# Performance work log

Measured on AMD Instinct MI355X. Metric: run time of the kernel, lower is better.

## Reference

```python
import jax, jax.numpy as jnp
import numpy as np

MAX_L = 6
L = MAX_L + 1  # internal self.max_l in the torch module
N = 2_000_000


def _sph_constants(Lmax):
    lm = np.arange(Lmax)
    ls = lm * lm
    pt = np.zeros((Lmax, Lmax), dtype=np.int64)
    yr = np.zeros((Lmax, Lmax), dtype=np.int64)
    yr_rev = np.zeros((Lmax, Lmax), dtype=np.int64)
    num_lm = (Lmax + 1) * Lmax // 2
    ca = np.zeros(num_lm, dtype=np.float64)
    cb = np.zeros(num_lm, dtype=np.float64)
    for l in range(Lmax):
        m = np.arange(l + 1)
        pt[l, : l + 1] = m + l * (l + 1) // 2
        yr[l, : l + 1] = ls[l] + l + m
        yr_rev[l, : l + 1] = ls[l] + l - m
        if l > 0:
            ca[pt[l, :l]] = np.sqrt((4.0 * ls[l] - 1.0) / (ls[l] - ls[:l]))
            cb[pt[l, :l]] = -np.sqrt((ls[l - 1] - ls[:l]) / (4.0 * ls[l - 1] - 1.0))
    p1 = -np.sqrt(1.0 + 0.5 / np.maximum(lm, 1))  # prefactor1; index 0 unused
    p2 = np.sqrt(2.0 * lm + 3.0)                  # prefactor2
    return pt, yr, yr_rev, ca, cb, p1, p2

_PT, _YR, _YRR, _CA, _CB, _P1, _P2 = _sph_constants(L)
_SQRT2_REV = float(np.sqrt(0.5))
_SQRT2PI_REV = float(np.sqrt(0.5 / np.pi))
_HC1 = float(np.sqrt(15.0 / (4.0 * np.pi)))
_HC2 = float(np.sqrt(5.0 / (16.0 * np.pi)))
_HC3 = float(np.sqrt(15.0 / (16.0 * np.pi)))


def setup_inputs() -> dict:
    key = jax.random.key(0)
    cart = jax.random.normal(key, (3, N), dtype=jnp.float32)
    return {"cart": cart}


def _sph_forward(cart):
    dt = cart.dtype
    x, y, z = cart[0], cart[1], cart[2]
    d_sq = x * x + y * y + z * z  # == norm(cart, axis=0)**2
    nb = x.ndim  # number of trailing batch dims (here 1)

    sph = [None] * (L * L)
    sph[0] = jnp.full(x.shape, _SQRT2PI_REV * _SQRT2_REV, dtype=dt)
    sph[1] = (_P1[1] * _SQRT2PI_REV) * y
    sph[2] = (_P2[0] * _SQRT2_REV * _SQRT2PI_REV) * z
    sph[3] = (_P1[1] * _SQRT2PI_REV) * x
    # l = 2 hard-coded block
    sph[4] = _HC1 * x * y
    sph[5] = -_HC1 * y * z
    sph[6] = _HC2 * (3.0 * z * z - d_sq)
    sph[7] = -_HC1 * x * z
    sph[8] = _HC3 * (x * x - y * y)

    for l in range(3, L):
        # vectorized band over m = 0..l-2 (positive-m / yr branch)
        a = jnp.asarray(_CA[_PT[l, : l - 1]], dt).reshape((l - 1,) + (1,) * nb)
        b = jnp.asarray(_CB[_PT[l, : l - 1]], dt).reshape((l - 1,) + (1,) * nb)
        prev = jnp.stack([sph[int(_YR[l - 1, m])] for m in range(l - 1)])
        prev2 = jnp.stack([sph[int(_YR[l - 2, m])] for m in range(l - 1)])
        blk = a * (z * prev + b * d_sq * prev2)
        for m in range(l - 1):
            sph[int(_YR[l, m])] = blk[m]
        # negative-m / yr_rev branch over m = 1..l-2
        if l - 1 > 1:
            a2 = jnp.asarray(_CA[_PT[l, 1 : l - 1]], dt).reshape((l - 2,) + (1,) * nb)
            b2 = jnp.asarray(_CB[_PT[l, 1 : l - 1]], dt).reshape((l - 2,) + (1,) * nb)
            prev_r = jnp.stack([sph[int(_YRR[l - 1, m])] for m in range(1, l - 1)])
            prev2_r = jnp.stack([sph[int(_YRR[l - 2, m])] for m in range(1, l - 1)])
            blk_r = a2 * (z * prev_r + b2 * d_sq * prev2_r)
            for i, m in enumerate(range(1, l - 1)):
                sph[int(_YRR[l, m])] = blk_r[i]
        # edge terms m = l-1 and m = l
        top_p = sph[int(_YR[l - 1, l - 1])]
        top_n = sph[int(_YRR[l - 1, l - 1])]
        sph[int(_YR[l, l - 1])] = _P2[l - 1] * z * top_p
        sph[int(_YRR[l, l - 1])] = _P2[l - 1] * z * top_n
        sph[int(_YR[l, l])] = _P1[l] * (x * top_p - y * top_n)
        sph[int(_YRR[l, l])] = _P1[l] * (x * top_n + y * top_p)

    return jnp.stack(sph)  # (L*L, ...batch)


def reference(cart):
    return _sph_forward(cart)
```

## Files before the change

kernel.cpp:

```cpp
#include <hip/hip_runtime.h>

constexpr double csqrt(double x) {
    double r = x > 1.0 ? x : 1.0;
    for (int i = 0; i < 60; ++i) r = 0.5 * (r + x / r);
    return r;
}

constexpr double PI_D    = 3.14159265358979323846264338327950288;
constexpr double SQ2R    = csqrt(0.5);
constexpr double SQ2PIR  = csqrt(0.5 / PI_D);
constexpr double C00_D   = SQ2PIR * SQ2R;
constexpr double C1Y_D   = -csqrt(1.5) * SQ2PIR;
constexpr double C1Z_D   = csqrt(3.0) * SQ2R * SQ2PIR;
constexpr double HC1_D   = csqrt(15.0 / (4.0 * PI_D));
constexpr double HC2_D   = csqrt(5.0 / (16.0 * PI_D));
constexpr double HC3_D   = csqrt(15.0 / (16.0 * PI_D));

struct SphConsts {
    double ca[7][7];
    double cb[7][7];
    double p1[7];
    double p2[7];
};

constexpr SphConsts makeConsts() {
    SphConsts c{};
    for (int l = 1; l < 7; ++l) {
        for (int m = 0; m < l; ++m) {
            c.ca[l][m] = csqrt((4.0 * l * l - 1.0) / (double)(l * l - m * m));
            double num = (double)((l - 1) * (l - 1) - m * m);
            double den = 4.0 * (l - 1) * (l - 1) - 1.0;
            c.cb[l][m] = -csqrt(num / den < 0.0 ? 0.0 : num / den);
        }
        c.p1[l] = -csqrt(1.0 + 0.5 / (double)l);
    }
    for (int l = 0; l < 7; ++l) c.p2[l] = csqrt(2.0 * l + 3.0);
    return c;
}

constexpr SphConsts CC = makeConsts();

typedef float f2 __attribute__((ext_vector_type(2)));

__device__ __forceinline__ void stv(float* p, float v) {
    __builtin_nontemporal_store(v, p);
}
__device__ __forceinline__ void stv(float* p, f2 v) {
    __builtin_nontemporal_store(v, reinterpret_cast<f2*>(p));
}

template <typename T> __device__ __forceinline__ T bcast(float v);
template <> __device__ __forceinline__ float bcast<float>(float v) { return v; }
template <> __device__ __forceinline__ f2    bcast<f2>(float v)    { f2 t = {v, v}; return t; }

template <typename T>
__device__ __forceinline__ void sph_point(T X, T Y, T Z, float* __restrict__ o, size_t N) {
    const T D = X * X + Y * Y + Z * Z;

    stv(o, bcast<T>((float)C00_D));
    T b1_0 = (float)C1Y_D * Y;
    T b1_1 = (float)C1Z_D * Z;
    T b1_2 = (float)C1Y_D * X;
    stv(o + 1 * N, b1_0);
    stv(o + 2 * N, b1_1);
    stv(o + 3 * N, b1_2);
    T b2_0 = (float)HC1_D * (X * Y);
    T b2_1 = (float)(-HC1_D) * (Y * Z);
    T b2_2 = (float)HC2_D * (3.0f * (Z * Z) - D);
    T b2_3 = (float)(-HC1_D) * (X * Z);
    T b2_4 = (float)HC3_D * (X * X - Y * Y);
    stv(o + 4 * N, b2_0);
    stv(o + 5 * N, b2_1);
    stv(o + 6 * N, b2_2);
    stv(o + 7 * N, b2_3);
    stv(o + 8 * N, b2_4);

    T prev2[13], prev[13], cur[13];
    prev2[0] = b1_0; prev2[1] = b1_1; prev2[2] = b1_2;
    prev[0] = b2_0; prev[1] = b2_1; prev[2] = b2_2; prev[3] = b2_3; prev[4] = b2_4;

#pragma unroll
    for (int l = 3; l <= 6; ++l) {
#pragma unroll
        for (int m = 0; m <= l - 2; ++m) {
            const float a = (float)CC.ca[l][m];
            const float b = (float)CC.cb[l][m];
            cur[l + m] = a * (Z * prev[(l - 1) + m] + b * (D * prev2[(l - 2) + m]));
        }
#pragma unroll
        for (int m = 1; m <= l - 2; ++m) {
            const float a = (float)CC.ca[l][m];
            const float b = (float)CC.cb[l][m];
            cur[l - m] = a * (Z * prev[(l - 1) - m] + b * (D * prev2[(l - 2) - m]));
        }
        const T top_p = prev[2 * l - 2];
        const T top_n = prev[0];
        const float p2v = (float)CC.p2[l - 1];
        const float p1v = (float)CC.p1[l];
        cur[2 * l - 1] = p2v * (Z * top_p);
        cur[1]         = p2v * (Z * top_n);
        cur[2 * l]     = p1v * (X * top_p - Y * top_n);
        cur[0]         = p1v * (X * top_n + Y * top_p);

#pragma unroll
        for (int j = 0; j <= 2 * l; ++j)
            stv(o + (size_t)(l * l + j) * N, cur[j]);

#pragma unroll
        for (int j = 0; j < 2 * l - 1; ++j) prev2[j] = prev[j];
#pragma unroll
        for (int j = 0; j < 2 * l + 1; ++j) prev[j] = cur[j];
    }
}

template <typename T, int W>
__global__ void sph_kernel(const float* __restrict__ cart,
                           float* __restrict__ out, int N) {
    const int i = blockIdx.x * blockDim.x + threadIdx.x;
    const int nW = N / W;
    if (i >= nW) return;
    const size_t sN = (size_t)N;
    const float* p = cart + (size_t)W * i;
    T X = *reinterpret_cast<const T*>(p);
    T Y = *reinterpret_cast<const T*>(p + sN);
    T Z = *reinterpret_cast<const T*>(p + 2 * sN);
    sph_point<T>(X, Y, Z, out + (size_t)W * i, sN);
}

extern "C" void kernel_launch(void* const* d_in, const int* in_sizes, int n_in,
                              void* d_out, int out_size, void* d_ws, size_t ws_size,
                              hipStream_t stream) {
    const float* cart = (const float*)d_in[0];
    float* out = (float*)d_out;
    const int N = in_sizes[0] / 3;

    const int threads = 256;
    if ((N & 1) == 0) {
        const int n2 = N >> 1;
        const int blocks = (n2 + threads - 1) / threads;
        sph_kernel<f2, 2><<<blocks, threads, 0, stream>>>(cart, out, N);
    } else {
        const int blocks = (N + threads - 1) / threads;
        sph_kernel<float, 1><<<blocks, threads, 0, stream>>>(cart, out, N);
    }
}
```

Before: 77.51 us.

## Reorder recurrence by m-columns and widen to float4 per thread

```diff
diff --git a/kernel.cpp b/kernel.cpp
--- a/kernel.cpp
+++ b/kernel.cpp
@@ -11,10 +11,6 @@
 constexpr double SQ2PIR  = csqrt(0.5 / PI_D);
 constexpr double C00_D   = SQ2PIR * SQ2R;
 constexpr double C1Y_D   = -csqrt(1.5) * SQ2PIR;
-constexpr double C1Z_D   = csqrt(3.0) * SQ2R * SQ2PIR;
-constexpr double HC1_D   = csqrt(15.0 / (4.0 * PI_D));
-constexpr double HC2_D   = csqrt(5.0 / (16.0 * PI_D));
-constexpr double HC3_D   = csqrt(15.0 / (16.0 * PI_D));
 
 struct SphConsts {
     double ca[7][7];
@@ -40,76 +36,73 @@
 
 constexpr SphConsts CC = makeConsts();
 
-typedef float f2 __attribute__((ext_vector_type(2)));
+typedef float f4 __attribute__((ext_vector_type(4)));
 
 __device__ __forceinline__ void stv(float* p, float v) {
     __builtin_nontemporal_store(v, p);
 }
-__device__ __forceinline__ void stv(float* p, f2 v) {
-    __builtin_nontemporal_store(v, reinterpret_cast<f2*>(p));
+__device__ __forceinline__ void stv(float* p, f4 v) {
+    __builtin_nontemporal_store(v, reinterpret_cast<f4*>(p));
 }
 
 template <typename T> __device__ __forceinline__ T bcast(float v);
 template <> __device__ __forceinline__ float bcast<float>(float v) { return v; }
-template <> __device__ __forceinline__ f2    bcast<f2>(float v)    { f2 t = {v, v}; return t; }
+template <> __device__ __forceinline__ f4    bcast<f4>(float v)    { f4 t = {v, v, v, v}; return t; }
 
 template <typename T>
-__device__ __forceinline__ void sph_point(T X, T Y, T Z, float* __restrict__ o, size_t N) {
-    const T D = X * X + Y * Y + Z * Z;
+__device__ __forceinline__ void sph_point(T x, T y, T z, float* __restrict__ o, size_t N) {
+    const T d2 = x * x + y * y + z * z;
 
-    stv(o, bcast<T>((float)C00_D));
-    T b1_0 = (float)C1Y_D * Y;
-    T b1_1 = (float)C1Z_D * Z;
-    T b1_2 = (float)C1Y_D * X;
-    stv(o + 1 * N, b1_0);
-    stv(o + 2 * N, b1_1);
-    stv(o + 3 * N, b1_2);
-    T b2_0 = (float)HC1_D * (X * Y);
-    T b2_1 = (float)(-HC1_D) * (Y * Z);
-    T b2_2 = (float)HC2_D * (3.0f * (Z * Z) - D);
-    T b2_3 = (float)(-HC1_D) * (X * Z);
-    T b2_4 = (float)HC3_D * (X * X - Y * Y);
-    stv(o + 4 * N, b2_0);
-    stv(o + 5 * N, b2_1);
-    stv(o + 6 * N, b2_2);
-    stv(o + 7 * N, b2_3);
-    stv(o + 8 * N, b2_4);
+    T pa = bcast<T>((float)C00_D);
+    stv(o + 0 * N, pa);
+    T pb = (float)CC.p2[0] * (z * pa);
+    stv(o + 2 * N, pb);
+#pragma unroll
+    for (int l = 2; l <= 6; ++l) {
+        const float a = (float)CC.ca[l][0];
+        const float b = (float)CC.cb[l][0];
+        T pc = a * (z * pb + b * (d2 * pa));
+        stv(o + (size_t)(l * l + l) * N, pc);
+        pa = pb; pb = pc;
+    }
 
-    T prev2[13], prev[13], cur[13];
-    prev2[0] = b1_0; prev2[1] = b1_1; prev2[2] = b1_2;
-    prev[0] = b2_0; prev[1] = b2_1; prev[2] = b2_2; prev[3] = b2_3; prev[4] = b2_4;
+    T dp = (float)C1Y_D * x;
+    T dn = (float)C1Y_D * y;
+    stv(o + 3 * N, dp);
+    stv(o + 1 * N, dn);
 
 #pragma unroll
-    for (int l = 3; l <= 6; ++l) {
+    for (int m = 1; m <= 6; ++m) {
+        if (m >= 2) {
+            const float p1v = (float)CC.p1[m];
+            T ndp = p1v * (x * dp - y * dn);
+            T ndn = p1v * (x * dn + y * dp);
+            dp = ndp; dn = ndn;
+            stv(o + (size_t)(m * m + 2 * m) * N, dp);
+            stv(o + (size_t)(m * m) * N, dn);
+        }
+        if (m <= 5) {
+            const float p2v = (float)CC.p2[m];
+            T qp = p2v * (z * dp);
+            T qn = p2v * (z * dn);
+            {
+                const int l = m + 1;
+                stv(o + (size_t)(l * l + l + m) * N, qp);
+                stv(o + (size_t)(l * l + l - m) * N, qn);
+            }
+            T ap = dp, bp = qp, an = dn, bn = qn;
 #pragma unroll
-        for (int m = 0; m <= l - 2; ++m) {
-            const float a = (float)CC.ca[l][m];
-            const float b = (float)CC.cb[l][m];
-            cur[l + m] = a * (Z * prev[(l - 1) + m] + b * (D * prev2[(l - 2) + m]));
+            for (int l = m + 2; l <= 6; ++l) {
+                const float a = (float)CC.ca[l][m];
+                const float b = (float)CC.cb[l][m];
+                T cp = a * (z * bp + b * (d2 * ap));
+                T cn = a * (z * bn + b * (d2 * an));
+                stv(o + (size_t)(l * l + l + m) * N, cp);
+                stv(o + (size_t)(l * l + l - m) * N, cn);
+                ap = bp; bp = cp;
+                an = bn; bn = cn;
+            }
         }
-#pragma unroll
-        for (int m = 1; m <= l - 2; ++m) {
-            const float a = (float)CC.ca[l][m];
-            const float b = (float)CC.cb[l][m];
-            cur[l - m] = a * (Z * prev[(l - 1) - m] + b * (D * prev2[(l - 2) - m]));
-        }
-        const T top_p = prev[2 * l - 2];
-        const T top_n = prev[0];
-        const float p2v = (float)CC.p2[l - 1];
-        const float p1v = (float)CC.p1[l];
-        cur[2 * l - 1] = p2v * (Z * top_p);
-        cur[1]         = p2v * (Z * top_n);
-        cur[2 * l]     = p1v * (X * top_p - Y * top_n);
-        cur[0]         = p1v * (X * top_n + Y * top_p);
-
-#pragma unroll
-        for (int j = 0; j <= 2 * l; ++j)
-            stv(o + (size_t)(l * l + j) * N, cur[j]);
-
-#pragma unroll
-        for (int j = 0; j < 2 * l - 1; ++j) prev2[j] = prev[j];
-#pragma unroll
-        for (int j = 0; j < 2 * l + 1; ++j) prev[j] = cur[j];
     }
 }
 
@@ -135,10 +128,10 @@
     const int N = in_sizes[0] / 3;
 
     const int threads = 256;
-    if ((N & 1) == 0) {
-        const int n2 = N >> 1;
-        const int blocks = (n2 + threads - 1) / threads;
-        sph_kernel<f2, 2><<<blocks, threads, 0, stream>>>(cart, out, N);
+    if ((N & 3) == 0) {
+        const int n4 = N >> 2;
+        const int blocks = (n4 + threads - 1) / threads;
+        sph_kernel<f4, 4><<<blocks, threads, 0, stream>>>(cart, out, N);
     } else {
         const int blocks = (N + threads - 1) / threads;
         sph_kernel<float, 1><<<blocks, threads, 0, stream>>>(cart, out, N);
```

Result: faster. 75.68 us, median of 2 (-2.4%).
